# Optimization experiments

Hardware: AMD Instinct MI355X
Metric: run time of the kernel (lower is better)

The kernel has to match this reference:

```python
import jax, jax.numpy as jnp
import numpy as np

FACTOR = 2
GAIN = 1.0

def _setup_fir(fir=(1, 3, 3, 1), gain=GAIN):
    k = np.asarray(fir, dtype=np.float32)
    if k.ndim == 1:
        k = np.outer(k, k)
    k = k / k.sum() * gain
    return k  # (4, 4)

def setup_inputs() -> dict:
    key = jax.random.key(0)
    kx, kw = jax.random.split(key)
    N, C, H, W = 16, 320, 64, 64
    x = jax.random.normal(kx, (N, C, H, W), dtype=jnp.float32)
    # variance-scaling uniform init (DDPM style): fan_in = fan_out = C*9
    fan = C * 3 * 3
    bound = float(np.sqrt(3.0 / fan))
    w = jax.random.uniform(kw, (C, C, 3, 3), dtype=jnp.float32, minval=-bound, maxval=bound)
    fir_k = jnp.asarray(_setup_fir())
    return {"x": x, "w": w, "fir_k": fir_k}

def reference(x, w, fir_k):
    # Fused FIR (upfirdn2d with up=1, down=1) + strided 3x3 conv downsample.
    C = x.shape[1]
    convW = w.shape[3]          # 3
    kH = fir_k.shape[0]         # 4
    p = kH - FACTOR + (convW - 1)           # 4
    pad0, pad1 = (p + 1) // 2, p // 2       # (2, 2)
    # upfirdn2d: zero-pad then true convolution (flipped kernel), depthwise
    xp = jnp.pad(x, ((0, 0), (0, 0), (pad0, pad1), (pad0, pad1)))
    kf = jnp.flip(fir_k, (0, 1))            # symmetric here, kept for faithfulness
    kd = jnp.broadcast_to(kf[None, None], (C, 1, kH, kH))
    y = jax.lax.conv_general_dilated(
        xp, kd, window_strides=(1, 1), padding='VALID',
        dimension_numbers=('NCHW', 'OIHW', 'NCHW'), feature_group_count=C)
    # strided conv2d, padding=0, stride=factor
    out = jax.lax.conv_general_dilated(
        y, w, window_strides=(FACTOR, FACTOR), padding='VALID',
        dimension_numbers=('NCHW', 'OIHW', 'NCHW'))
    return out  # [N, C, H//2, W//2]
```

## Files before the change

kernel.cpp:

```cpp
#include <hip/hip_runtime.h>
#include <hip/hip_bf16.h>


typedef short bf16x8_t __attribute__((ext_vector_type(8)));
typedef float f32x4 __attribute__((ext_vector_type(4)));
typedef unsigned int u32x4 __attribute__((ext_vector_type(4)));
typedef __attribute__((address_space(1))) const unsigned int* as1_u32p;
typedef __attribute__((address_space(3))) unsigned int* as3_u32p;

#define NI 16
#define CCH 320
#define HW 64
#define HY 65
#define HY2 4225
#define CCSTEP 135200

__global__ __launch_bounds__(256) void fir_kernel(const float* __restrict__ x,
                                                  const float* __restrict__ fir_k,
                                                  __hip_bfloat16* __restrict__ yt) {
    __shared__ float vlds[4 * 32 * 69];
    int bx = blockIdx.x;
    int n    = bx / 170;
    int rem  = bx % 170;
    int band = rem / 10;
    int cc   = rem % 10;
    int r0   = band * 4;

    float f0 = fir_k[0] + fir_k[1] + fir_k[2] + fir_k[3];
    float f1 = fir_k[4] + fir_k[5] + fir_k[6] + fir_k[7];
    float f2 = fir_k[8] + fir_k[9] + fir_k[10] + fir_k[11];
    float f3 = fir_k[12] + fir_k[13] + fir_k[14] + fir_k[15];

    int tid = threadIdx.x;
    int lane = tid & 63;
    int g = tid >> 6;

    for (int cis = g; cis < 32; cis += 4) {
        int ci = cc * 32 + cis;
        const float* xb = x + (size_t)(n * CCH + ci) * HW * HW;
        float xr[7];
#pragma unroll
        for (int t = 0; t < 7; ++t) {
            int row = r0 + t - 2;
            xr[t] = (row >= 0 && row < HW) ? xb[row * HW + lane] : 0.f;
        }
#pragma unroll
        for (int j = 0; j < 4; ++j) {
            float v = f0 * xr[j] + f1 * xr[j + 1] + f2 * xr[j + 2] + f3 * xr[j + 3];
            float* vrow = vlds + (j * 32 + cis) * 69;
            vrow[lane + 2] = v;
            if (lane < 2)   vrow[lane] = 0.f;
            if (lane >= 62) vrow[lane + 4] = 0.f;
        }
    }
    __syncthreads();

    unsigned short* yu = (unsigned short*)yt;
    int s  = tid & 3;
    int pl = tid >> 2;
    size_t plane = (size_t)(n * 10 + cc) * HY2;
#pragma unroll
    for (int it = 0; it < 5; ++it) {
        int pid = it * 64 + pl;
        if (pid < 260) {
            int j = pid / 65;
            int c = pid % 65;
            int r = r0 + j;
            if (r < HY) {
                const float* vb = vlds + (j * 32 + s * 8) * 69 + c;
                float a[8];
#pragma unroll
                for (int k = 0; k < 8; ++k) {
                    const float* vr = vb + k * 69;
                    a[k] = f0 * vr[0] + f1 * vr[1] + f2 * vr[2] + f3 * vr[3];
                }
                unsigned int wd[4];
#pragma unroll
                for (int h = 0; h < 4; ++h) {
                    unsigned int lo = __bfloat16_as_ushort(__float2bfloat16(a[2 * h]));
                    unsigned int hi = __bfloat16_as_ushort(__float2bfloat16(a[2 * h + 1]));
                    wd[h] = lo | (hi << 16);
                }
                *(u32x4*)(yu + (plane + (size_t)r * HY + c) * 32 + s * 8) =
                    (u32x4){wd[0], wd[1], wd[2], wd[3]};
            }
        }
    }
}

__global__ __launch_bounds__(256) void wt2_kernel(const float* __restrict__ w,
                                                  __hip_bfloat16* __restrict__ wt) {
    int idx = blockIdx.x * 256 + threadIdx.x;
    if (idx < 9 * CCH * CCH) {
        int j  = idx & 7;
        int co = (idx >> 3) % CCH;
        int t2 = idx / 2560;
        int q  = t2 & 3;
        int cc = (t2 >> 2) % 10;
        int tap = t2 / 40;
        int ci = cc * 32 + q * 8 + j;
        wt[idx] = __float2bfloat16(w[(co * CCH + ci) * 9 + tap]);
    }
}

__global__ __launch_bounds__(256, 3) void conv_kernel(const __hip_bfloat16* __restrict__ yt,
                                                      const __hip_bfloat16* __restrict__ wt2,
                                                      float* __restrict__ out) {
    __shared__ short ylds[2][1536 * 8];

    int bx = blockIdx.x;
    int sp = bx & 15;
    int t  = bx >> 4;
    int cb = t % 5;
    int n  = t / 5;
    int co0 = cb * 64;
    int oh0 = (sp >> 1) * 4;
    int ow0 = (sp & 1) * 16;

    int tid = threadIdx.x;
    int lane = tid & 63;
    int wid = tid >> 6;
    int q = lane >> 4, lc = lane & 15;

    const unsigned short* ytu = (const unsigned short*)yt;
    const unsigned short* wtu = (const unsigned short*)wt2;

    int ybase = (n * 10 * HY2 + (2 * oh0) * HY + 2 * ow0) * 32;
    int goff[6];
#pragma unroll
    for (int k = 0; k < 6; ++k) {
        int u = k * 256 + tid;
        int uc = (u < 1485) ? u : 1484;
        int p = uc / 5, s = uc - p * 5;
        if (s == 4) s = 3;
        int pr = p / 33, pc = p - pr * 33;
        goff[k] = ybase + (pr * HY + pc) * 32 + s * 8;
    }

    const unsigned short* wbl = wtu + q * 2560 + (size_t)(co0 + wid * 16 + lc) * 8;
    const int aoff = (2 * lc) * 40 + q * 8;

    f32x4 acc[4];
#pragma unroll
    for (int i = 0; i < 4; ++i) acc[i] = (f32x4){0.f, 0.f, 0.f, 0.f};

    bf16x8_t bfr[2][9];

#define GLDS(buf, K, ccidx)                                                            \
    __builtin_amdgcn_global_load_lds(                                                  \
        (as1_u32p)(ytu + goff[K] + (ccidx) * CCSTEP),                                  \
        (as3_u32p)(&ylds[buf][(size_t)((K) * 256 + wid * 64) * 8]), 16, 0, 0)

#pragma unroll
    for (int k = 0; k < 6; ++k) GLDS(0, k, 0);
#pragma unroll
    for (int kk = 0; kk < 9; ++kk)
        bfr[0][kk] = *(const bf16x8_t*)(wbl + kk * 102400);
    __syncthreads();

    auto compute = [&](const short* buf, const bf16x8_t* b) {
#pragma unroll
        for (int kw = 0; kw < 3; ++kw) {
            bf16x8_t af[9];
#pragma unroll
            for (int r = 0; r < 9; ++r)
                af[r] = *(const bf16x8_t*)(buf + aoff + (r * 33 + kw) * 40);
#pragma unroll
            for (int kh = 0; kh < 3; ++kh)
#pragma unroll
                for (int mf = 0; mf < 4; ++mf)
                    acc[mf] = __builtin_amdgcn_mfma_f32_16x16x32_bf16(
                        b[kh * 3 + kw], af[2 * mf + kh], acc[mf], 0, 0, 0);
        }
    };

    for (int tt = 0; tt < 5; ++tt) {
        int cc0 = 2 * tt, cc1 = 2 * tt + 1;
        {
#pragma unroll
            for (int k = 0; k < 6; ++k) GLDS(1, k, cc0 + 1);
            const unsigned short* wnx = wbl + (cc0 + 1) * 10240;
#pragma unroll
            for (int kk = 0; kk < 9; ++kk)
                bfr[1][kk] = *(const bf16x8_t*)(wnx + kk * 102400);
            compute(&ylds[0][0], bfr[0]);
            __syncthreads();
        }
        {
            if (cc1 < 9) {
#pragma unroll
                for (int k = 0; k < 6; ++k) GLDS(0, k, cc1 + 1);
                const unsigned short* wnx = wbl + (cc1 + 1) * 10240;
#pragma unroll
                for (int kk = 0; kk < 9; ++kk)
                    bfr[0][kk] = *(const bf16x8_t*)(wnx + kk * 102400);
            }
            compute(&ylds[1][0], bfr[1]);
            if (cc1 < 9) __syncthreads();
        }
    }
#undef GLDS

#pragma unroll
    for (int mf = 0; mf < 4; ++mf) {
        int oh = oh0 + mf;
        int ow = ow0 + lc;
#pragma unroll
        for (int rg = 0; rg < 4; ++rg) {
            int co = co0 + wid * 16 + q * 4 + rg;
            out[((n * CCH + co) * 32 + oh) * 32 + ow] = acc[mf][rg];
        }
    }
}

__global__ __launch_bounds__(256) void naive_kernel(const float* __restrict__ x,
                                                    const float* __restrict__ w,
                                                    const float* __restrict__ fk,
                                                    float* __restrict__ out) {
    int idx = blockIdx.x * 256 + threadIdx.x;
    if (idx >= NI * CCH * 32 * 32) return;
    int ow = idx & 31;
    int oh = (idx >> 5) & 31;
    int co = (idx >> 10) % CCH;
    int n = (idx >> 10) / CCH;
    float f0 = fk[0] + fk[1] + fk[2] + fk[3];
    float f1 = fk[4] + fk[5] + fk[6] + fk[7];
    float f2 = fk[8] + fk[9] + fk[10] + fk[11];
    float f3 = fk[12] + fk[13] + fk[14] + fk[15];
    float fv[4] = {f0, f1, f2, f3};
    float acc = 0.f;
    for (int ci = 0; ci < CCH; ++ci) {
        const float* xb = x + (size_t)(n * CCH + ci) * HW * HW;
        const float* wb = w + (size_t)(co * CCH + ci) * 9;
#pragma unroll
        for (int u = 0; u < 3; ++u) {
            int yr = 2 * oh + u;
#pragma unroll
            for (int v = 0; v < 3; ++v) {
                int yc = 2 * ow + v;
                float s = 0.f;
#pragma unroll
                for (int a = 0; a < 4; ++a) {
                    int xrw = yr - 2 + a;
                    if (xrw < 0 || xrw >= HW) continue;
                    float t = 0.f;
#pragma unroll
                    for (int b = 0; b < 4; ++b) {
                        int xc = yc - 2 + b;
                        if (xc >= 0 && xc < HW) t += fv[b] * xb[xrw * HW + xc];
                    }
                    s += fv[a] * t;
                }
                acc += wb[u * 3 + v] * s;
            }
        }
    }
    out[idx] = acc;
}

extern "C" void kernel_launch(void* const* d_in, const int* in_sizes, int n_in,
                              void* d_out, int out_size, void* d_ws, size_t ws_size,
                              hipStream_t stream) {
    const float* x = (const float*)d_in[0];
    const float* w = (const float*)d_in[1];
    const float* fk = (const float*)d_in[2];
    float* out = (float*)d_out;

    const size_t ybytes = (size_t)NI * 10 * HY2 * 32 * 2;
    const size_t wtoff = ybytes;
    const size_t need = wtoff + (size_t)9 * CCH * CCH * 2;

    if (ws_size >= need) {
        __hip_bfloat16* yt = (__hip_bfloat16*)d_ws;
        __hip_bfloat16* wt = (__hip_bfloat16*)((char*)d_ws + wtoff);
        fir_kernel<<<16 * 17 * 10, 256, 0, stream>>>(x, fk, yt);
        wt2_kernel<<<(9 * CCH * CCH + 255) / 256, 256, 0, stream>>>(w, wt);
        conv_kernel<<<16 * 5 * 16, 256, 0, stream>>>(yt, wt, out);
    } else {
        naive_kernel<<<(NI * CCH * 32 * 32 + 255) / 256, 256, 0, stream>>>(x, w, fk, out);
    }
}
```

Measured before the change: 76.42 us.

## Restructure conv to 2-wave blocks with 32 channels per wave and streamed weights

The conv kernel now runs 128 threads per block, and each wave computes 32 output channels with two N-fragments. Each A fragment read from LDS is therefore reused across twice as many MFMAs. Weight fragments are prefetched one kw slice at a time instead of holding all 9 taps double-buffered, which cuts register pressure, and the channel-chunk loop becomes a simple double-buffered loop with the LDS prefetch issued before compute. The FIR kernel stores its vertical intermediate in LDS as bf16 and has each thread produce two adjacent output columns, roughly halving LDS traffic. This adds a bf16 rounding of the intermediate, and fewer waves per block may reduce latency hiding.

```diff
diff --git a/kernel.cpp b/kernel.cpp
--- a/kernel.cpp
+++ b/kernel.cpp
@@ -18,7 +18,7 @@
 __global__ __launch_bounds__(256) void fir_kernel(const float* __restrict__ x,
                                                   const float* __restrict__ fir_k,
                                                   __hip_bfloat16* __restrict__ yt) {
-    __shared__ float vlds[4 * 32 * 69];
+    __shared__ unsigned short vlds[4 * 32 * 70];
     int bx = blockIdx.x;
     int n    = bx / 170;
     int rem  = bx % 170;
@@ -47,42 +47,62 @@
 #pragma unroll
         for (int j = 0; j < 4; ++j) {
             float v = f0 * xr[j] + f1 * xr[j + 1] + f2 * xr[j + 2] + f3 * xr[j + 3];
-            float* vrow = vlds + (j * 32 + cis) * 69;
-            vrow[lane + 2] = v;
-            if (lane < 2)   vrow[lane] = 0.f;
-            if (lane >= 62) vrow[lane + 4] = 0.f;
+            unsigned short* vrow = vlds + (j * 32 + cis) * 70;
+            vrow[lane + 2] = __bfloat16_as_ushort(__float2bfloat16(v));
+            if (lane < 2)   vrow[lane] = 0;
+            if (lane >= 62) vrow[lane + 4] = 0;
         }
     }
     __syncthreads();
 
     unsigned short* yu = (unsigned short*)yt;
-    int s  = tid & 3;
-    int pl = tid >> 2;
     size_t plane = (size_t)(n * 10 + cc) * HY2;
 #pragma unroll
-    for (int it = 0; it < 5; ++it) {
-        int pid = it * 64 + pl;
-        if (pid < 260) {
-            int j = pid / 65;
-            int c = pid % 65;
-            int r = r0 + j;
+    for (int it = 0; it < 3; ++it) {
+        int task = it * 256 + tid;
+        if (task < 528) {
+            int s  = task & 3;
+            int t2 = task >> 2;
+            int j  = t2 / 33;
+            int pp = t2 % 33;
+            int c  = 2 * pp;
+            int r  = r0 + j;
             if (r < HY) {
-                const float* vb = vlds + (j * 32 + s * 8) * 69 + c;
-                float a[8];
+                const unsigned short* vb = vlds + (j * 32 + s * 8) * 70 + c;
+                bool pair = (pp < 32);
+                float a0[8], a1[8];
 #pragma unroll
                 for (int k = 0; k < 8; ++k) {
-                    const float* vr = vb + k * 69;
-                    a[k] = f0 * vr[0] + f1 * vr[1] + f2 * vr[2] + f3 * vr[3];
+                    const unsigned short* vr = vb + k * 70;
+                    float v0 = __bfloat162float(__ushort_as_bfloat16(vr[0]));
+                    float v1 = __bfloat162float(__ushort_as_bfloat16(vr[1]));
+                    float v2 = __bfloat162float(__ushort_as_bfloat16(vr[2]));
+                    float v3 = __bfloat162float(__ushort_as_bfloat16(vr[3]));
+                    a0[k] = f0 * v0 + f1 * v1 + f2 * v2 + f3 * v3;
+                    if (pair) {
+                        float v4 = __bfloat162float(__ushort_as_bfloat16(vr[4]));
+                        a1[k] = f0 * v1 + f1 * v2 + f2 * v3 + f3 * v4;
+                    }
                 }
-                unsigned int wd[4];
+                unsigned int w0[4];
 #pragma unroll
                 for (int h = 0; h < 4; ++h) {
-                    unsigned int lo = __bfloat16_as_ushort(__float2bfloat16(a[2 * h]));
-                    unsigned int hi = __bfloat16_as_ushort(__float2bfloat16(a[2 * h + 1]));
-                    wd[h] = lo | (hi << 16);
+                    unsigned int lo = __bfloat16_as_ushort(__float2bfloat16(a0[2 * h]));
+                    unsigned int hi = __bfloat16_as_ushort(__float2bfloat16(a0[2 * h + 1]));
+                    w0[h] = lo | (hi << 16);
                 }
-                *(u32x4*)(yu + (plane + (size_t)r * HY + c) * 32 + s * 8) =
-                    (u32x4){wd[0], wd[1], wd[2], wd[3]};
+                size_t base = (plane + (size_t)r * HY + c) * 32 + s * 8;
+                *(u32x4*)(yu + base) = (u32x4){w0[0], w0[1], w0[2], w0[3]};
+                if (pair) {
+                    unsigned int w1[4];
+#pragma unroll
+                    for (int h = 0; h < 4; ++h) {
+                        unsigned int lo = __bfloat16_as_ushort(__float2bfloat16(a1[2 * h]));
+                        unsigned int hi = __bfloat16_as_ushort(__float2bfloat16(a1[2 * h + 1]));
+                        w1[h] = lo | (hi << 16);
+                    }
+                    *(u32x4*)(yu + base + 32) = (u32x4){w1[0], w1[1], w1[2], w1[3]};
+                }
             }
         }
     }
@@ -103,9 +123,9 @@
     }
 }
 
-__global__ __launch_bounds__(256, 3) void conv_kernel(const __hip_bfloat16* __restrict__ yt,
-                                                      const __hip_bfloat16* __restrict__ wt2,
-                                                      float* __restrict__ out) {
+__global__ __launch_bounds__(128) void conv_kernel(const __hip_bfloat16* __restrict__ yt,
+                                                   const __hip_bfloat16* __restrict__ wt2,
+                                                   float* __restrict__ out) {
     __shared__ short ylds[2][1536 * 8];
 
     int bx = blockIdx.x;
@@ -126,10 +146,10 @@
     const unsigned short* wtu = (const unsigned short*)wt2;
 
     int ybase = (n * 10 * HY2 + (2 * oh0) * HY + 2 * ow0) * 32;
-    int goff[6];
-#pragma unroll
-    for (int k = 0; k < 6; ++k) {
-        int u = k * 256 + tid;
+    int goff[12];
+#pragma unroll
+    for (int k = 0; k < 12; ++k) {
+        int u = k * 128 + tid;
         int uc = (u < 1485) ? u : 1484;
         int p = uc / 5, s = uc - p * 5;
         if (s == 4) s = 3;
@@ -137,78 +157,82 @@
         goff[k] = ybase + (pr * HY + pc) * 32 + s * 8;
     }
 
-    const unsigned short* wbl = wtu + q * 2560 + (size_t)(co0 + wid * 16 + lc) * 8;
+    const unsigned short* wbl = wtu + q * 2560 + (size_t)(co0 + wid * 32 + lc) * 8;
     const int aoff = (2 * lc) * 40 + q * 8;
 
-    f32x4 acc[4];
-#pragma unroll
-    for (int i = 0; i < 4; ++i) acc[i] = (f32x4){0.f, 0.f, 0.f, 0.f};
-
-    bf16x8_t bfr[2][9];
+    f32x4 acc[4][2];
+#pragma unroll
+    for (int i = 0; i < 4; ++i)
+#pragma unroll
+        for (int j = 0; j < 2; ++j) acc[i][j] = (f32x4){0.f, 0.f, 0.f, 0.f};
+
+    bf16x8_t bq[6];
 
 #define GLDS(buf, K, ccidx)                                                            \
     __builtin_amdgcn_global_load_lds(                                                  \
         (as1_u32p)(ytu + goff[K] + (ccidx) * CCSTEP),                                  \
-        (as3_u32p)(&ylds[buf][(size_t)((K) * 256 + wid * 64) * 8]), 16, 0, 0)
-
-#pragma unroll
-    for (int k = 0; k < 6; ++k) GLDS(0, k, 0);
-#pragma unroll
-    for (int kk = 0; kk < 9; ++kk)
-        bfr[0][kk] = *(const bf16x8_t*)(wbl + kk * 102400);
+        (as3_u32p)(&ylds[buf][(size_t)((K) * 128 + wid * 64) * 8]), 16, 0, 0)
+
+#define LOADB(dst, ccidx, kw)                                                          \
+    {                                                                                  \
+        const unsigned short* wcc_ = wbl + (ccidx) * 10240;                            \
+        _Pragma("unroll")                                                              \
+        for (int kh_ = 0; kh_ < 3; ++kh_)                                              \
+            _Pragma("unroll")                                                          \
+            for (int nf_ = 0; nf_ < 2; ++nf_)                                          \
+                dst[kh_ * 2 + nf_] = *(const bf16x8_t*)(wcc_ + (kh_ * 3 + (kw)) * 102400 + nf_ * 128); \
+    }
+
+#pragma unroll
+    for (int k = 0; k < 12; ++k) GLDS(0, k, 0);
+    LOADB(bq, 0, 0);
     __syncthreads();
 
-    auto compute = [&](const short* buf, const bf16x8_t* b) {
+    for (int cc = 0; cc < 10; ++cc) {
+        const short* buf = &ylds[cc & 1][0];
+        if (cc < 9) {
+#pragma unroll
+            for (int k = 0; k < 12; ++k) GLDS((cc & 1) ^ 1, k, cc + 1);
+        }
 #pragma unroll
         for (int kw = 0; kw < 3; ++kw) {
             bf16x8_t af[9];
 #pragma unroll
             for (int r = 0; r < 9; ++r)
                 af[r] = *(const bf16x8_t*)(buf + aoff + (r * 33 + kw) * 40);
+            bf16x8_t bn[6];
+            if (kw < 2) {
+                LOADB(bn, cc, kw + 1);
+            } else if (cc < 9) {
+                LOADB(bn, cc + 1, 0);
+            }
 #pragma unroll
             for (int kh = 0; kh < 3; ++kh)
 #pragma unroll
                 for (int mf = 0; mf < 4; ++mf)
-                    acc[mf] = __builtin_amdgcn_mfma_f32_16x16x32_bf16(
-                        b[kh * 3 + kw], af[2 * mf + kh], acc[mf], 0, 0, 0);
-        }
-    };
-
-    for (int tt = 0; tt < 5; ++tt) {
-        int cc0 = 2 * tt, cc1 = 2 * tt + 1;
-        {
-#pragma unroll
-            for (int k = 0; k < 6; ++k) GLDS(1, k, cc0 + 1);
-            const unsigned short* wnx = wbl + (cc0 + 1) * 10240;
-#pragma unroll
-            for (int kk = 0; kk < 9; ++kk)
-                bfr[1][kk] = *(const bf16x8_t*)(wnx + kk * 102400);
-            compute(&ylds[0][0], bfr[0]);
-            __syncthreads();
-        }
-        {
-            if (cc1 < 9) {
-#pragma unroll
-                for (int k = 0; k < 6; ++k) GLDS(0, k, cc1 + 1);
-                const unsigned short* wnx = wbl + (cc1 + 1) * 10240;
-#pragma unroll
-                for (int kk = 0; kk < 9; ++kk)
-                    bfr[0][kk] = *(const bf16x8_t*)(wnx + kk * 102400);
-            }
-            compute(&ylds[1][0], bfr[1]);
-            if (cc1 < 9) __syncthreads();
-        }
+#pragma unroll
+                    for (int nf = 0; nf < 2; ++nf)
+                        acc[mf][nf] = __builtin_amdgcn_mfma_f32_16x16x32_bf16(
+                            bq[kh * 2 + nf], af[2 * mf + kh], acc[mf][nf], 0, 0, 0);
+#pragma unroll
+            for (int i = 0; i < 6; ++i) bq[i] = bn[i];
+        }
+        __syncthreads();
     }
 #undef GLDS
+#undef LOADB
 
 #pragma unroll
     for (int mf = 0; mf < 4; ++mf) {
         int oh = oh0 + mf;
         int ow = ow0 + lc;
 #pragma unroll
-        for (int rg = 0; rg < 4; ++rg) {
-            int co = co0 + wid * 16 + q * 4 + rg;
-            out[((n * CCH + co) * 32 + oh) * 32 + ow] = acc[mf][rg];
+        for (int nf = 0; nf < 2; ++nf) {
+#pragma unroll
+            for (int rg = 0; rg < 4; ++rg) {
+                int co = co0 + wid * 32 + nf * 16 + q * 4 + rg;
+                out[((n * CCH + co) * 32 + oh) * 32 + ow] = acc[mf][nf][rg];
+            }
         }
     }
 }
@@ -275,7 +299,7 @@
         __hip_bfloat16* wt = (__hip_bfloat16*)((char*)d_ws + wtoff);
         fir_kernel<<<16 * 17 * 10, 256, 0, stream>>>(x, fk, yt);
         wt2_kernel<<<(9 * CCH * CCH + 255) / 256, 256, 0, stream>>>(w, wt);
-        conv_kernel<<<16 * 5 * 16, 256, 0, stream>>>(yt, wt, out);
+        conv_kernel<<<16 * 5 * 16, 128, 0, stream>>>(yt, wt, out);
     } else {
         naive_kernel<<<(NI * CCH * 32 * 32 + 255) / 256, 256, 0, stream>>>(x, w, fk, out);
     }
```

After: 103.2 us. 1.35x slower.
